# Kernel optimization log

Measured on AMD Instinct MI355X. Metric: run time of the kernel, lower is better.

## Reference

```python
import jax, jax.numpy as jnp
import numpy as np

VOCAB, B, T, E, H, C = 50000, 1024, 120, 50, 300, 5
FORGET_BIAS = 1.0  # tf.nn.rnn_cell.LSTMCell default


def setup_inputs() -> dict:
    key = jax.random.key(0)
    ks = jax.random.split(key, 8)
    tokens = jax.random.randint(ks[0], (B, T, 1), 0, VOCAB, dtype=jnp.int32)
    labels = jax.random.randint(ks[1], (B, T), 0, C, dtype=jnp.int32)
    mask = jax.random.randint(ks[2], (B, T), 0, 2, dtype=jnp.int32).astype(bool)
    embeddings = jax.random.normal(ks[3], (VOCAB, E), dtype=jnp.float32) * 0.1
    Wx = jax.random.normal(ks[4], (E, 4 * H), dtype=jnp.float32) * (1.0 / np.sqrt(E))
    Wh = jax.random.normal(ks[5], (H, 4 * H), dtype=jnp.float32) * (1.0 / np.sqrt(H))
    b = jnp.zeros((4 * H,), dtype=jnp.float32)
    U = jax.random.normal(ks[6], (H, C), dtype=jnp.float32) * (1.0 / np.sqrt(H))
    b2 = jnp.zeros((C,), dtype=jnp.float32)
    return {"tokens": tokens, "labels": labels, "mask": mask,
            "embeddings": embeddings, "Wx": Wx, "Wh": Wh, "b": b, "U": U, "b2": b2}


def reference(tokens, labels, mask, embeddings, Wx, Wh, b, U, b2):
    # Embedding lookup: (B, T, n_features=1) -> (B, T, E)
    x = embeddings[tokens[..., 0]]

    def step(carry, xt):
        c, h = carry
        z = xt @ Wx + h @ Wh + b           # (B, 4H), gate order i, j, f, o
        i, j, f, o = jnp.split(z, 4, axis=-1)
        c_new = jax.nn.sigmoid(f + FORGET_BIAS) * c + jax.nn.sigmoid(i) * jnp.tanh(j)
        h_new = jax.nn.sigmoid(o) * jnp.tanh(c_new)
        return (c_new, h_new), h_new

    nb = x.shape[0]
    c0 = jnp.zeros((nb, H), dtype=x.dtype)
    h0 = jnp.zeros((nb, H), dtype=x.dtype)
    _, hs = jax.lax.scan(step, (c0, h0), jnp.swapaxes(x, 0, 1))  # (T, B, H)
    hs = jnp.swapaxes(hs, 0, 1)                                   # (B, T, H)

    logits = hs @ U + b2                                          # (B, T, C)
    logp = jax.nn.log_softmax(logits, axis=-1)
    ce = -jnp.take_along_axis(logp, labels[..., None].astype(jnp.int32), axis=-1)[..., 0]
    m = mask.astype(ce.dtype)
    loss = jnp.sum(ce * m) / jnp.sum(m)  # mean over unmasked tokens
    return loss
```

## Files before the change

kernel.cpp:

```cpp
#include <hip/hip_runtime.h>
#include <hip/hip_bf16.h>
#include <math.h>

#define NBATCH 1024
#define NT 120
#define NE 50
#define NH 300
#define NC 5
#define GH 1200
#define NKPAD 352
#define NSTRIP 15
#define HS 20
#define SCOL 80
#define NGRP 16
#define BB 64
#define ASTR 376
#define WSTR 376
#define ZSTR 84
#define HBSTR 304
#define HCH 76
#define NCHUNK 4800

typedef __attribute__((ext_vector_type(8))) short short8;
typedef __attribute__((ext_vector_type(4))) float f32x4;
typedef __attribute__((ext_vector_type(2))) unsigned short us2;

static __device__ __forceinline__ float bf2f(unsigned short u) {
    unsigned int x = ((unsigned int)u) << 16;
    return __builtin_bit_cast(float, x);
}
static __device__ __forceinline__ unsigned short f2bf(float f) {
    __hip_bfloat16 h = __float2bfloat16(f);
    return __builtin_bit_cast(unsigned short, h);
}

static __device__ __forceinline__ float sigmoid_fast(float x) {
    return __builtin_amdgcn_rcpf(1.f + __expf(-x));
}
static __device__ __forceinline__ float tanh_fast(float x) {
    return 1.f - 2.f * __builtin_amdgcn_rcpf(1.f + __expf(2.f * x));
}

__global__ __launch_bounds__(256)
void wswz_kernel(const float* __restrict__ Wx, const float* __restrict__ Wh,
                 unsigned short* __restrict__ Wswz)
{
    int idx = blockIdx.x * 256 + threadIdx.x;
    if (idx >= NSTRIP * SCOL * NKPAD) return;
    int s = idx / (SCOL * NKPAD);
    int r = idx % (SCOL * NKPAD);
    int j = r / NKPAD, k = r % NKPAD;
    int col = (j & 3) * NH + s * HS + (j >> 2);
    float v = 0.f;
    if (k < NH)           v = Wh[k * GH + col];
    else if (k < NH + NE) v = Wx[(k - NH) * GH + col];
    Wswz[idx] = f2bf(v);
}

__device__ __forceinline__ void load_h(const unsigned short* __restrict__ hb,
                                       int b0, unsigned short* A_s, int tid)
{
    const unsigned long long* src =
        (const unsigned long long*)(hb + (size_t)b0 * HBSTR);
    unsigned long long v[19];
#pragma unroll
    for (int m = 0; m < 19; ++m) {
        const int idx = tid + 256 * m;
        if (idx < NCHUNK) {
            const int row = idx / 75, j = idx % 75;
            v[m] = __hip_atomic_load(src + (size_t)row * HCH + j,
                                     __ATOMIC_RELAXED, __HIP_MEMORY_SCOPE_AGENT);
        }
    }
#pragma unroll
    for (int m = 0; m < 19; ++m) {
        const int idx = tid + 256 * m;
        if (idx < NCHUNK) {
            const int row = idx / 75, j = idx % 75;
            *(unsigned long long*)(A_s + row * ASTR + j * 4) = v[m];
        }
    }
}

__device__ __forceinline__ void store_h(unsigned short* hb, int b0, int st,
                                        const unsigned short* h_stage, int tid)
{
#pragma unroll
    for (int m = 0; m < 2; ++m) {
        const int c = tid + m * 256;
        if (c < 320) {
            const int row = c / 5, j = c % 5;
            unsigned long long val =
                *(const unsigned long long*)(h_stage + row * HS + j * 4);
            unsigned long long* p = (unsigned long long*)
                (hb + (size_t)(b0 + row) * HBSTR + st * HS + j * 4);
            __hip_atomic_store(p, val, __ATOMIC_RELAXED,
                               __HIP_MEMORY_SCOPE_AGENT);
        }
    }
}

__device__ __forceinline__ void load_x(const int* __restrict__ tokens,
                                       const float* __restrict__ emb,
                                       int b0, int t, unsigned short* A_s, int tid)
{
    const int row = tid >> 2, q = tid & 3;
    const int tok = tokens[(b0 + row) * NT + t];
    const float* er = emb + (size_t)tok * NE;
    unsigned short* dst = A_s + row * ASTR + NH;
    for (int m = 0; m < 7; ++m) {
        int f = q + 4 * m;
        if (f < 25) {
            float2 v = *(const float2*)(er + f * 2);
            us2 o; o.x = f2bf(v.x); o.y = f2bf(v.y);
            *(us2*)(dst + f * 2) = o;
        }
    }
}

__device__ __forceinline__ void ce_phase0(bool doCE, int r0, int nr,
        const unsigned short* A_s, const float* U_s, float* llds, int tid)
{
    if (!doCE || tid >= 192) return;
    for (int item = tid; item < nr * 50; item += 192) {
        int i = item / 50, rem = item % 50, c = rem / 10, q = rem % 10;
        const unsigned short* ar = A_s + (r0 + i) * ASTR + q * 30;
        const float* up = U_s + q * 30 * NC + c;
        float acc = 0.f;
#pragma unroll
        for (int k = 0; k < 30; ++k) acc += bf2f(ar[k]) * up[k * NC];
        llds[i * 50 + c * 10 + q] = acc;
    }
}

__device__ __forceinline__ void ce_final(bool doCE, int tc, int b0, int r0,
        int nr, const float* b2r, const int* __restrict__ labels,
        const int* __restrict__ mask, float* __restrict__ ce_arr,
        const float* llds, int tid)
{
    if (!doCE || tid >= nr) return;
    const float* pp = llds + tid * 50;
    float L[5];
#pragma unroll
    for (int c = 0; c < 5; ++c) {
        float sum = 0.f;
#pragma unroll
        for (int q = 0; q < 10; ++q) sum += pp[c * 10 + q];
        L[c] = sum + b2r[c];
    }
    float m = fmaxf(fmaxf(fmaxf(L[0], L[1]), fmaxf(L[2], L[3])), L[4]);
    float ssum = expf(L[0]-m)+expf(L[1]-m)+expf(L[2]-m)+expf(L[3]-m)+expf(L[4]-m);
    float lse = m + logf(ssum);
    int bidx = b0 + r0 + tid;
    int lab = labels[bidx * NT + tc];
    int mk  = mask[bidx * NT + tc];
    ce_arr[bidx * NT + tc] = mk ? (lse - L[lab]) : 0.f;
}

__global__ __launch_bounds__(256, 1)
void lstm_persist(const int* __restrict__ tokens,
                  const int* __restrict__ labels,
                  const int* __restrict__ mask,
                  const float* __restrict__ emb,
                  const float* __restrict__ bias,
                  const float* __restrict__ U,
                  const float* __restrict__ b2,
                  const unsigned short* __restrict__ Wswz,
                  unsigned short* __restrict__ hbuf,
                  float* __restrict__ ce_arr,
                  int* __restrict__ flags)
{
    __shared__ unsigned short A_s[BB * ASTR];
    __shared__ unsigned short W_s[SCOL * WSTR];
    __shared__ __align__(16) unsigned short h_stage[BB * HS];
    __shared__ float z_s[BB * ZSTR];
    __shared__ float c_s[BB * HS];
    __shared__ float U_s[NH * NC];
    __shared__ float b_s[SCOL];
    __shared__ float llds[5 * 50];

    const int tid  = threadIdx.x;
    const int g    = blockIdx.x & 15;
    const int s    = blockIdx.x >> 4;
    const int b0   = g * BB;
    const int wave = tid >> 6;
    const int lane = tid & 63;
    const int c15  = lane & 15;
    const int kq   = lane >> 4;
    const int r0   = (s * BB) / NSTRIP;
    const int r1   = ((s + 1) * BB) / NSTRIP;
    const int nr   = r1 - r0;

    for (int idx = tid; idx < SCOL * 44; idx += 256) {
        int j = idx / 44, ch = idx % 44;
        *(uint4*)(W_s + j * WSTR + ch * 8) =
            *(const uint4*)(Wswz + (size_t)s * SCOL * NKPAD + j * NKPAD + ch * 8);
    }
    for (int idx = tid; idx < BB * NH; idx += 256) {
        int row = idx / NH, k = idx % NH;
        A_s[row * ASTR + k] = 0;
    }
    for (int idx = tid; idx < BB * 26; idx += 256) {
        int row = idx / 26, k = 350 + idx % 26;
        A_s[row * ASTR + k] = 0;
    }
    for (int idx = tid; idx < BB * HS; idx += 256) c_s[idx] = 0.f;
    for (int idx = tid; idx < NH * NC; idx += 256) U_s[idx] = U[idx];
    if (tid < SCOL) b_s[tid] = bias[(tid & 3) * NH + s * HS + (tid >> 2)];
    float b2r[5];
#pragma unroll
    for (int c = 0; c < 5; ++c) b2r[c] = b2[c];
    load_x(tokens, emb, b0, 0, A_s, tid);
    __syncthreads();

    const unsigned short* Ab = A_s + (wave * 16 + c15) * ASTR + kq * 8;
    const unsigned short* Wb = W_s + c15 * WSTR + kq * 8;

    for (int t = 0; t < NT; ++t) {
        f32x4 acc[5];
#pragma unroll
        for (int n = 0; n < 5; ++n) acc[n] = (f32x4){0.f, 0.f, 0.f, 0.f};
#pragma unroll
        for (int ks = 0; ks < 11; ++ks) {
            short8 av = *(const short8*)(Ab + ks * 32);
#pragma unroll
            for (int n = 0; n < 5; ++n) {
                short8 bv = *(const short8*)(Wb + n * 16 * WSTR + ks * 32);
                acc[n] = __builtin_amdgcn_mfma_f32_16x16x32_bf16(av, bv, acc[n], 0, 0, 0);
            }
        }
#pragma unroll
        for (int n = 0; n < 5; ++n)
#pragma unroll
            for (int j = 0; j < 4; ++j)
                z_s[(wave * 16 + kq * 4 + j) * ZSTR + n * 16 + c15] = acc[n][j];
        __syncthreads();

        if (t + 1 < NT) load_x(tokens, emb, b0, t + 1, A_s, tid);
#pragma unroll
        for (int ii = 0; ii < 5; ++ii) {
            int idx = tid * 5 + ii;
            int row = idx / HS, h = idx % HS;
            f32x4 z4 = *(f32x4*)(z_s + row * ZSTR + h * 4);
            float zi = z4[0] + b_s[4 * h + 0];
            float zj = z4[1] + b_s[4 * h + 1];
            float zf = z4[2] + b_s[4 * h + 2];
            float zo = z4[3] + b_s[4 * h + 3];
            float co = c_s[idx];
            float fg = sigmoid_fast(zf + 1.f);
            float ig = sigmoid_fast(zi);
            float og = sigmoid_fast(zo);
            float cn = fg * co + ig * tanh_fast(zj);
            float hn = og * tanh_fast(cn);
            c_s[idx] = cn;
            h_stage[idx] = f2bf(hn);
        }
        __syncthreads();

        unsigned short* hb = hbuf + (size_t)(t & 1) * (NBATCH * HBSTR);
        store_h(hb, b0, s, h_stage, tid);
        ce_phase0(t >= 1, r0, nr, A_s, U_s, llds, tid);
        asm volatile("s_waitcnt vmcnt(0)" ::: "memory");
        __syncthreads();

        if (tid == 0)
            __hip_atomic_store(flags + (size_t)(t * NGRP + g) * 16 + s, 1,
                               __ATOMIC_RELAXED, __HIP_MEMORY_SCOPE_AGENT);
        if (tid >= 192) {
            if (tid < 192 + NSTRIP) {
                const int* fp = flags + (size_t)(t * NGRP + g) * 16 + (tid - 192);
                int fv = 0; int gu = 0;
                do {
                    fv = __hip_atomic_load(fp, __ATOMIC_RELAXED,
                                           __HIP_MEMORY_SCOPE_AGENT);
                    if (!fv) __builtin_amdgcn_s_sleep(1);
                } while (!fv && ++gu < (1 << 17));
            }
        } else {
            ce_final(t >= 1, t - 1, b0, r0, nr, b2r, labels, mask,
                     ce_arr, llds, tid);
        }
        __syncthreads();

        load_h(hb, b0, A_s, tid);
        __syncthreads();
    }

    ce_phase0(true, r0, nr, A_s, U_s, llds, tid);
    __syncthreads();
    ce_final(true, NT - 1, b0, r0, nr, b2r, labels, mask, ce_arr, llds, tid);
}

__global__ __launch_bounds__(256)
void reduce1_kernel(const float* __restrict__ ce_arr,
                    const int* __restrict__ mask,
                    float* __restrict__ pce, float* __restrict__ pm)
{
    __shared__ float s_ce[256];
    __shared__ float s_m[256];
    const int tid = threadIdx.x;
    const int lo = blockIdx.x * 480;
    float ac = 0.f, am = 0.f;
    for (int i = lo + tid; i < lo + 480; i += 256) {
        ac += ce_arr[i];
        am += (float)mask[i];
    }
    s_ce[tid] = ac; s_m[tid] = am;
    __syncthreads();
    for (int r = 128; r > 0; r >>= 1) {
        if (tid < r) { s_ce[tid] += s_ce[tid + r]; s_m[tid] += s_m[tid + r]; }
        __syncthreads();
    }
    if (tid == 0) { pce[blockIdx.x] = s_ce[0]; pm[blockIdx.x] = s_m[0]; }
}

__global__ __launch_bounds__(256)
void reduce2_kernel(const float* __restrict__ pce,
                    const float* __restrict__ pm,
                    float* __restrict__ out)
{
    __shared__ float s_ce[256];
    __shared__ float s_m[256];
    const int tid = threadIdx.x;
    s_ce[tid] = pce[tid];
    s_m[tid]  = pm[tid];
    __syncthreads();
    for (int r = 128; r > 0; r >>= 1) {
        if (tid < r) { s_ce[tid] += s_ce[tid + r]; s_m[tid] += s_m[tid + r]; }
        __syncthreads();
    }
    if (tid == 0) out[0] = s_ce[0] / s_m[0];
}

extern "C" void kernel_launch(void* const* d_in, const int* in_sizes, int n_in,
                              void* d_out, int out_size, void* d_ws, size_t ws_size,
                              hipStream_t stream)
{
    const int*   tokens = (const int*)d_in[0];
    const int*   labels = (const int*)d_in[1];
    const int*   mask   = (const int*)d_in[2];
    const float* emb    = (const float*)d_in[3];
    const float* Wx     = (const float*)d_in[4];
    const float* Wh     = (const float*)d_in[5];
    const float* bias   = (const float*)d_in[6];
    const float* U      = (const float*)d_in[7];
    const float* b2     = (const float*)d_in[8];

    char* wsb = (char*)d_ws;
    unsigned short* Wswz = (unsigned short*)wsb;
    unsigned short* hbuf = (unsigned short*)(wsb + 844800);
    float* ce    = (float*)(wsb + 2089984);
    float* pce   = (float*)(wsb + 2581504);
    float* pm    = (float*)(wsb + 2582528);
    int*   flags = (int*)(wsb + 2583552);

    hipMemsetAsync(flags, 0, 122880, stream);
    wswz_kernel<<<(NSTRIP * SCOL * NKPAD + 255) / 256, 256, 0, stream>>>(Wx, Wh, Wswz);
    lstm_persist<<<NGRP * NSTRIP, 256, 0, stream>>>(
        tokens, labels, mask, emb, bias, U, b2, Wswz, hbuf, ce, flags);
    reduce1_kernel<<<256, 256, 0, stream>>>(ce, mask, pce, pm);
    reduce2_kernel<<<1, 256, 0, stream>>>(pce, pm, (float*)d_out);
}
```

Before: 670.1 us.

## Replace block-wide barriers with per-wave decoupled sync and wave-level flags

Each wave now owns 16 batch rows end to end: it writes z, runs the gate math, stores its h slice, publishes a per-wave monotonic step counter, and polls only the matching waves of the other strips before reloading its own h rows. All __syncthreads in the time loop become wave-local LDS waits. The cross-entropy projection is fused into a per-wave shuffle reduction, and the per-step flag array is replaced by counters, which shrinks the memset. This removes block barriers and lets waves progress independently, at the cost of 4x more flag traffic and polling. Ordering of h stores relative to flag stores still relies on an explicit vmcnt wait with relaxed atomics.

```diff
diff --git a/kernel.cpp b/kernel.cpp
--- a/kernel.cpp
+++ b/kernel.cpp
@@ -19,10 +19,11 @@
 #define ZSTR 84
 #define HBSTR 304
 #define HCH 76
-#define NCHUNK 4800
+typedef unsigned long long ull;
 
 typedef __attribute__((ext_vector_type(8))) short short8;
 typedef __attribute__((ext_vector_type(4))) float f32x4;
+typedef __attribute__((ext_vector_type(4))) unsigned short us4;
 typedef __attribute__((ext_vector_type(2))) unsigned short us2;
 
 static __device__ __forceinline__ float bf2f(unsigned short u) {
@@ -33,13 +34,15 @@
     __hip_bfloat16 h = __float2bfloat16(f);
     return __builtin_bit_cast(unsigned short, h);
 }
-
 static __device__ __forceinline__ float sigmoid_fast(float x) {
     return __builtin_amdgcn_rcpf(1.f + __expf(-x));
 }
 static __device__ __forceinline__ float tanh_fast(float x) {
     return 1.f - 2.f * __builtin_amdgcn_rcpf(1.f + __expf(2.f * x));
 }
+#define LGKM_FENCE() do { \
+    asm volatile("s_waitcnt lgkmcnt(0)" ::: "memory"); \
+    __builtin_amdgcn_sched_barrier(0); } while (0)
 
 __global__ __launch_bounds__(256)
 void wswz_kernel(const float* __restrict__ Wx, const float* __restrict__ Wh,
@@ -57,57 +60,15 @@
     Wswz[idx] = f2bf(v);
 }
 
-__device__ __forceinline__ void load_h(const unsigned short* __restrict__ hb,
-                                       int b0, unsigned short* A_s, int tid)
-{
-    const unsigned long long* src =
-        (const unsigned long long*)(hb + (size_t)b0 * HBSTR);
-    unsigned long long v[19];
-#pragma unroll
-    for (int m = 0; m < 19; ++m) {
-        const int idx = tid + 256 * m;
-        if (idx < NCHUNK) {
-            const int row = idx / 75, j = idx % 75;
-            v[m] = __hip_atomic_load(src + (size_t)row * HCH + j,
-                                     __ATOMIC_RELAXED, __HIP_MEMORY_SCOPE_AGENT);
-        }
-    }
-#pragma unroll
-    for (int m = 0; m < 19; ++m) {
-        const int idx = tid + 256 * m;
-        if (idx < NCHUNK) {
-            const int row = idx / 75, j = idx % 75;
-            *(unsigned long long*)(A_s + row * ASTR + j * 4) = v[m];
-        }
-    }
-}
-
-__device__ __forceinline__ void store_h(unsigned short* hb, int b0, int st,
-                                        const unsigned short* h_stage, int tid)
-{
-#pragma unroll
-    for (int m = 0; m < 2; ++m) {
-        const int c = tid + m * 256;
-        if (c < 320) {
-            const int row = c / 5, j = c % 5;
-            unsigned long long val =
-                *(const unsigned long long*)(h_stage + row * HS + j * 4);
-            unsigned long long* p = (unsigned long long*)
-                (hb + (size_t)(b0 + row) * HBSTR + st * HS + j * 4);
-            __hip_atomic_store(p, val, __ATOMIC_RELAXED,
-                               __HIP_MEMORY_SCOPE_AGENT);
-        }
-    }
-}
-
-__device__ __forceinline__ void load_x(const int* __restrict__ tokens,
-                                       const float* __restrict__ emb,
-                                       int b0, int t, unsigned short* A_s, int tid)
-{
-    const int row = tid >> 2, q = tid & 3;
+__device__ __forceinline__ void load_x_wave(const int* __restrict__ tokens,
+        const float* __restrict__ emb, int b0, int w, int t,
+        unsigned short* A_s, int lane)
+{
+    const int row = w * 16 + (lane >> 2), q = lane & 3;
     const int tok = tokens[(b0 + row) * NT + t];
     const float* er = emb + (size_t)tok * NE;
     unsigned short* dst = A_s + row * ASTR + NH;
+#pragma unroll
     for (int m = 0; m < 7; ++m) {
         int f = q + 4 * m;
         if (f < 25) {
@@ -118,43 +79,89 @@
     }
 }
 
-__device__ __forceinline__ void ce_phase0(bool doCE, int r0, int nr,
-        const unsigned short* A_s, const float* U_s, float* llds, int tid)
-{
-    if (!doCE || tid >= 192) return;
-    for (int item = tid; item < nr * 50; item += 192) {
-        int i = item / 50, rem = item % 50, c = rem / 10, q = rem % 10;
-        const unsigned short* ar = A_s + (r0 + i) * ASTR + q * 30;
-        const float* up = U_s + q * 30 * NC + c;
-        float acc = 0.f;
-#pragma unroll
-        for (int k = 0; k < 30; ++k) acc += bf2f(ar[k]) * up[k * NC];
-        llds[i * 50 + c * 10 + q] = acc;
-    }
-}
-
-__device__ __forceinline__ void ce_final(bool doCE, int tc, int b0, int r0,
-        int nr, const float* b2r, const int* __restrict__ labels,
-        const int* __restrict__ mask, float* __restrict__ ce_arr,
-        const float* llds, int tid)
-{
-    if (!doCE || tid >= nr) return;
-    const float* pp = llds + tid * 50;
-    float L[5];
-#pragma unroll
-    for (int c = 0; c < 5; ++c) {
-        float sum = 0.f;
-#pragma unroll
-        for (int q = 0; q < 10; ++q) sum += pp[c * 10 + q];
-        L[c] = sum + b2r[c];
-    }
-    float m = fmaxf(fmaxf(fmaxf(L[0], L[1]), fmaxf(L[2], L[3])), L[4]);
-    float ssum = expf(L[0]-m)+expf(L[1]-m)+expf(L[2]-m)+expf(L[3]-m)+expf(L[4]-m);
-    float lse = m + logf(ssum);
-    int bidx = b0 + r0 + tid;
-    int lab = labels[bidx * NT + tc];
-    int mk  = mask[bidx * NT + tc];
-    ce_arr[bidx * NT + tc] = mk ? (lse - L[lab]) : 0.f;
+__device__ __forceinline__ void store_h_wave(unsigned short* hb, int b0,
+        int s, int w, const unsigned short* h_stage, int lane)
+{
+#pragma unroll
+    for (int m = 0; m < 2; ++m) {
+        const int c = lane + 64 * m;
+        if (c < 80) {
+            const int rl = c / 5, j = c % 5;
+            ull val = *(const ull*)(h_stage + (w * 16 + rl) * HS + j * 4);
+            ull* p = (ull*)(hb + (size_t)(b0 + w * 16 + rl) * HBSTR
+                            + s * HS + j * 4);
+            __hip_atomic_store(p, val, __ATOMIC_RELAXED,
+                               __HIP_MEMORY_SCOPE_AGENT);
+        }
+    }
+}
+
+__device__ __forceinline__ void load_h_wave(const unsigned short* __restrict__ hb,
+        int b0, int w, unsigned short* A_s, int lane)
+{
+    const ull* src = (const ull*)hb;
+    ull v[19];
+#pragma unroll
+    for (int m = 0; m < 19; ++m) {
+        const int idx = lane + 64 * m;
+        if (idx < 1200) {
+            const int rl = idx / 75, j = idx % 75;
+            v[m] = __hip_atomic_load(src + (size_t)(b0 + w * 16 + rl) * HCH + j,
+                                     __ATOMIC_RELAXED, __HIP_MEMORY_SCOPE_AGENT);
+        }
+    }
+#pragma unroll
+    for (int m = 0; m < 19; ++m) {
+        const int idx = lane + 64 * m;
+        if (idx < 1200) {
+            const int rl = idx / 75, j = idx % 75;
+            *(ull*)(A_s + (w * 16 + rl) * ASTR + j * 4) = v[m];
+        }
+    }
+}
+
+__device__ __forceinline__ void ce_wave(bool doCE, int tc, int b0, int lo,
+        int hi, const unsigned short* A_s, const float* U_s,
+        const float* b2r, const int* __restrict__ labels,
+        const int* __restrict__ mask, float* __restrict__ ce_arr, int lane)
+{
+    if (!doCE || lo >= hi) return;
+    const int ridx = lane >> 2, part = lane & 3;
+    const int row = lo + ridx;
+    const bool act = (row < hi) && (ridx < hi - lo);
+    float L0 = 0.f, L1 = 0.f, L2 = 0.f, L3 = 0.f, L4 = 0.f;
+    if (act) {
+        const int k0 = part * 76;
+        const int n4 = (part < 3) ? 19 : 18;
+        const unsigned short* ar = A_s + row * ASTR + k0;
+        for (int c4 = 0; c4 < n4; ++c4) {
+            us4 hv4 = *(const us4*)(ar + c4 * 4);
+#pragma unroll
+            for (int e = 0; e < 4; ++e) {
+                float hv = bf2f(hv4[e]);
+                const float* up = U_s + (k0 + c4 * 4 + e) * NC;
+                L0 += hv * up[0]; L1 += hv * up[1]; L2 += hv * up[2];
+                L3 += hv * up[3]; L4 += hv * up[4];
+            }
+        }
+    }
+    L0 += __shfl_xor(L0, 1, 64); L0 += __shfl_xor(L0, 2, 64);
+    L1 += __shfl_xor(L1, 1, 64); L1 += __shfl_xor(L1, 2, 64);
+    L2 += __shfl_xor(L2, 1, 64); L2 += __shfl_xor(L2, 2, 64);
+    L3 += __shfl_xor(L3, 1, 64); L3 += __shfl_xor(L3, 2, 64);
+    L4 += __shfl_xor(L4, 1, 64); L4 += __shfl_xor(L4, 2, 64);
+    if (act && part == 0) {
+        float L[5] = { L0 + b2r[0], L1 + b2r[1], L2 + b2r[2],
+                       L3 + b2r[3], L4 + b2r[4] };
+        float m = fmaxf(fmaxf(fmaxf(L[0], L[1]), fmaxf(L[2], L[3])), L[4]);
+        float ssum = expf(L[0]-m)+expf(L[1]-m)+expf(L[2]-m)
+                   + expf(L[3]-m)+expf(L[4]-m);
+        float lse = m + logf(ssum);
+        int bidx = b0 + row;
+        int lab = labels[bidx * NT + tc];
+        int mk  = mask[bidx * NT + tc];
+        ce_arr[bidx * NT + tc] = mk ? (lse - L[lab]) : 0.f;
+    }
 }
 
 __global__ __launch_bounds__(256, 1)
@@ -177,19 +184,19 @@
     __shared__ float c_s[BB * HS];
     __shared__ float U_s[NH * NC];
     __shared__ float b_s[SCOL];
-    __shared__ float llds[5 * 50];
 
     const int tid  = threadIdx.x;
     const int g    = blockIdx.x & 15;
     const int s    = blockIdx.x >> 4;
     const int b0   = g * BB;
-    const int wave = tid >> 6;
+    const int w    = tid >> 6;
     const int lane = tid & 63;
     const int c15  = lane & 15;
     const int kq   = lane >> 4;
     const int r0   = (s * BB) / NSTRIP;
     const int r1   = ((s + 1) * BB) / NSTRIP;
-    const int nr   = r1 - r0;
+    const int lo   = max(r0, w * 16);
+    const int hi   = min(r1, w * 16 + 16);
 
     for (int idx = tid; idx < SCOL * 44; idx += 256) {
         int j = idx / 44, ch = idx % 44;
@@ -210,10 +217,10 @@
     float b2r[5];
 #pragma unroll
     for (int c = 0; c < 5; ++c) b2r[c] = b2[c];
-    load_x(tokens, emb, b0, 0, A_s, tid);
+    load_x_wave(tokens, emb, b0, w, 0, A_s, lane);
     __syncthreads();
 
-    const unsigned short* Ab = A_s + (wave * 16 + c15) * ASTR + kq * 8;
+    const unsigned short* Ab = A_s + (w * 16 + c15) * ASTR + kq * 8;
     const unsigned short* Wb = W_s + c15 * WSTR + kq * 8;
 
     for (int t = 0; t < NT; ++t) {
@@ -233,62 +240,66 @@
         for (int n = 0; n < 5; ++n)
 #pragma unroll
             for (int j = 0; j < 4; ++j)
-                z_s[(wave * 16 + kq * 4 + j) * ZSTR + n * 16 + c15] = acc[n][j];
-        __syncthreads();
-
-        if (t + 1 < NT) load_x(tokens, emb, b0, t + 1, A_s, tid);
+                z_s[(w * 16 + kq * 4 + j) * ZSTR + n * 16 + c15] = acc[n][j];
+        LGKM_FENCE();
+
+        if (t + 1 < NT) load_x_wave(tokens, emb, b0, w, t + 1, A_s, lane);
+
 #pragma unroll
         for (int ii = 0; ii < 5; ++ii) {
-            int idx = tid * 5 + ii;
-            int row = idx / HS, h = idx % HS;
-            f32x4 z4 = *(f32x4*)(z_s + row * ZSTR + h * 4);
+            int idxl = lane * 5 + ii;
+            int rl = idxl / HS, h = idxl % HS;
+            int grow = w * 16 + rl;
+            f32x4 z4 = *(f32x4*)(z_s + grow * ZSTR + h * 4);
             float zi = z4[0] + b_s[4 * h + 0];
             float zj = z4[1] + b_s[4 * h + 1];
             float zf = z4[2] + b_s[4 * h + 2];
             float zo = z4[3] + b_s[4 * h + 3];
-            float co = c_s[idx];
+            int cidx = w * 320 + idxl;
+            float co = c_s[cidx];
             float fg = sigmoid_fast(zf + 1.f);
             float ig = sigmoid_fast(zi);
             float og = sigmoid_fast(zo);
             float cn = fg * co + ig * tanh_fast(zj);
             float hn = og * tanh_fast(cn);
-            c_s[idx] = cn;
-            h_stage[idx] = f2bf(hn);
-        }
-        __syncthreads();
+            c_s[cidx] = cn;
+            h_stage[cidx] = f2bf(hn);
+        }
+        LGKM_FENCE();
 
         unsigned short* hb = hbuf + (size_t)(t & 1) * (NBATCH * HBSTR);
-        store_h(hb, b0, s, h_stage, tid);
-        ce_phase0(t >= 1, r0, nr, A_s, U_s, llds, tid);
+        store_h_wave(hb, b0, s, w, h_stage, lane);
         asm volatile("s_waitcnt vmcnt(0)" ::: "memory");
-        __syncthreads();
-
-        if (tid == 0)
-            __hip_atomic_store(flags + (size_t)(t * NGRP + g) * 16 + s, 1,
+
+        if (lane == 0)
+            __hip_atomic_store(flags + g * 64 + s * 4 + w, t + 1,
                                __ATOMIC_RELAXED, __HIP_MEMORY_SCOPE_AGENT);
-        if (tid >= 192) {
-            if (tid < 192 + NSTRIP) {
-                const int* fp = flags + (size_t)(t * NGRP + g) * 16 + (tid - 192);
-                int fv = 0; int gu = 0;
-                do {
-                    fv = __hip_atomic_load(fp, __ATOMIC_RELAXED,
-                                           __HIP_MEMORY_SCOPE_AGENT);
-                    if (!fv) __builtin_amdgcn_s_sleep(1);
-                } while (!fv && ++gu < (1 << 17));
+
+        ce_wave(t >= 1, t - 1, b0, lo, hi, A_s, U_s, b2r,
+                labels, mask, ce_arr, lane);
+
+        {
+            const int* fbase = flags + g * 64 + w;
+            int done = (lane >= NSTRIP);
+            int gu = 0;
+            while (true) {
+                if (!done) {
+                    int fv = __hip_atomic_load(fbase + lane * 4,
+                                               __ATOMIC_RELAXED,
+                                               __HIP_MEMORY_SCOPE_AGENT);
+                    done = (fv >= t + 1);
+                }
+                if (__ballot(done) == ~0ull) break;
+                if (++gu > (1 << 20)) break;
+                __builtin_amdgcn_s_sleep(2);
             }
-        } else {
-            ce_final(t >= 1, t - 1, b0, r0, nr, b2r, labels, mask,
-                     ce_arr, llds, tid);
-        }
-        __syncthreads();
-
-        load_h(hb, b0, A_s, tid);
-        __syncthreads();
-    }
-
-    ce_phase0(true, r0, nr, A_s, U_s, llds, tid);
-    __syncthreads();
-    ce_final(true, NT - 1, b0, r0, nr, b2r, labels, mask, ce_arr, llds, tid);
+        }
+
+        load_h_wave(hb, b0, w, A_s, lane);
+        LGKM_FENCE();
+    }
+
+    ce_wave(true, NT - 1, b0, lo, hi, A_s, U_s, b2r, labels, mask, ce_arr, lane);
 }
 
 __global__ __launch_bounds__(256)
@@ -354,7 +365,7 @@
     float* pm    = (float*)(wsb + 2582528);
     int*   flags = (int*)(wsb + 2583552);
 
-    hipMemsetAsync(flags, 0, 122880, stream);
+    hipMemsetAsync(flags, 0, 4096, stream);
     wswz_kernel<<<(NSTRIP * SCOL * NKPAD + 255) / 256, 256, 0, stream>>>(Wx, Wh, Wswz);
     lstm_persist<<<NGRP * NSTRIP, 256, 0, stream>>>(
         tokens, labels, mask, emb, bias, U, b2, Wswz, hbuf, ce, flags);
```

Result: slower. 1.188 ms (+77.3%).

## Overlap per-strip flag waits with h loads and copy own strip locally

Applied to the files above, without the earlier changes.

The old step waited on all 15 strip flags, hit a barrier, then had every thread load the whole hidden state. Now each 16-thread group handles one strip. It waits on that strip's flag (one lane polls and broadcasts) and loads that strip's h slice into shared memory as soon as it is ready. The block's own strip is copied directly from h_stage without a global round trip. This removes a barrier and overlaps slow-arriving strips with loads of ready ones. It moves the CE final work to the last 16 threads, which assumes nr never exceeds 16, and raises the spin limit.

```diff
diff --git a/kernel.cpp b/kernel.cpp
--- a/kernel.cpp
+++ b/kernel.cpp
@@ -18,8 +18,7 @@
 #define WSTR 376
 #define ZSTR 84
 #define HBSTR 304
-#define HCH 76
-#define NCHUNK 4800
+typedef unsigned long long ull;
 
 typedef __attribute__((ext_vector_type(8))) short short8;
 typedef __attribute__((ext_vector_type(4))) float f32x4;
@@ -33,7 +32,6 @@
     __hip_bfloat16 h = __float2bfloat16(f);
     return __builtin_bit_cast(unsigned short, h);
 }
-
 static __device__ __forceinline__ float sigmoid_fast(float x) {
     return __builtin_amdgcn_rcpf(1.f + __expf(-x));
 }
@@ -57,31 +55,6 @@
     Wswz[idx] = f2bf(v);
 }
 
-__device__ __forceinline__ void load_h(const unsigned short* __restrict__ hb,
-                                       int b0, unsigned short* A_s, int tid)
-{
-    const unsigned long long* src =
-        (const unsigned long long*)(hb + (size_t)b0 * HBSTR);
-    unsigned long long v[19];
-#pragma unroll
-    for (int m = 0; m < 19; ++m) {
-        const int idx = tid + 256 * m;
-        if (idx < NCHUNK) {
-            const int row = idx / 75, j = idx % 75;
-            v[m] = __hip_atomic_load(src + (size_t)row * HCH + j,
-                                     __ATOMIC_RELAXED, __HIP_MEMORY_SCOPE_AGENT);
-        }
-    }
-#pragma unroll
-    for (int m = 0; m < 19; ++m) {
-        const int idx = tid + 256 * m;
-        if (idx < NCHUNK) {
-            const int row = idx / 75, j = idx % 75;
-            *(unsigned long long*)(A_s + row * ASTR + j * 4) = v[m];
-        }
-    }
-}
-
 __device__ __forceinline__ void store_h(unsigned short* hb, int b0, int st,
                                         const unsigned short* h_stage, int tid)
 {
@@ -90,10 +63,8 @@
         const int c = tid + m * 256;
         if (c < 320) {
             const int row = c / 5, j = c % 5;
-            unsigned long long val =
-                *(const unsigned long long*)(h_stage + row * HS + j * 4);
-            unsigned long long* p = (unsigned long long*)
-                (hb + (size_t)(b0 + row) * HBSTR + st * HS + j * 4);
+            ull val = *(const ull*)(h_stage + row * HS + j * 4);
+            ull* p = (ull*)(hb + (size_t)(b0 + row) * HBSTR + st * HS + j * 4);
             __hip_atomic_store(p, val, __ATOMIC_RELAXED,
                                __HIP_MEMORY_SCOPE_AGENT);
         }
@@ -136,10 +107,10 @@
 __device__ __forceinline__ void ce_final(bool doCE, int tc, int b0, int r0,
         int nr, const float* b2r, const int* __restrict__ labels,
         const int* __restrict__ mask, float* __restrict__ ce_arr,
-        const float* llds, int tid)
-{
-    if (!doCE || tid >= nr) return;
-    const float* pp = llds + tid * 50;
+        const float* llds, int idx)
+{
+    if (!doCE || idx >= nr) return;
+    const float* pp = llds + idx * 50;
     float L[5];
 #pragma unroll
     for (int c = 0; c < 5; ++c) {
@@ -151,7 +122,7 @@
     float m = fmaxf(fmaxf(fmaxf(L[0], L[1]), fmaxf(L[2], L[3])), L[4]);
     float ssum = expf(L[0]-m)+expf(L[1]-m)+expf(L[2]-m)+expf(L[3]-m)+expf(L[4]-m);
     float lse = m + logf(ssum);
-    int bidx = b0 + r0 + tid;
+    int bidx = b0 + r0 + idx;
     int lab = labels[bidx * NT + tc];
     int mk  = mask[bidx * NT + tc];
     ce_arr[bidx * NT + tc] = mk ? (lse - L[lab]) : 0.f;
@@ -190,6 +161,8 @@
     const int r0   = (s * BB) / NSTRIP;
     const int r1   = ((s + 1) * BB) / NSTRIP;
     const int nr   = r1 - r0;
+    const int sp   = tid >> 4;
+    const int kk   = tid & 15;
 
     for (int idx = tid; idx < SCOL * 44; idx += 256) {
         int j = idx / 44, ch = idx % 44;
@@ -266,23 +239,48 @@
         if (tid == 0)
             __hip_atomic_store(flags + (size_t)(t * NGRP + g) * 16 + s, 1,
                                __ATOMIC_RELAXED, __HIP_MEMORY_SCOPE_AGENT);
-        if (tid >= 192) {
-            if (tid < 192 + NSTRIP) {
-                const int* fp = flags + (size_t)(t * NGRP + g) * 16 + (tid - 192);
+        if (tid < 240) {
+            if (sp == s) {
+#pragma unroll
+                for (int r4 = 0; r4 < 4; ++r4) {
+                    int row = kk * 4 + r4;
+#pragma unroll
+                    for (int j = 0; j < 5; ++j)
+                        *(ull*)(A_s + row * ASTR + s * HS + j * 4) =
+                            *(const ull*)(h_stage + row * HS + j * 4);
+                }
+            } else {
+                const int lead = lane & ~15;
+                const int* fp = flags + (size_t)(t * NGRP + g) * 16 + sp;
                 int fv = 0; int gu = 0;
                 do {
-                    fv = __hip_atomic_load(fp, __ATOMIC_RELAXED,
-                                           __HIP_MEMORY_SCOPE_AGENT);
-                    if (!fv) __builtin_amdgcn_s_sleep(1);
-                } while (!fv && ++gu < (1 << 17));
+                    int lv = 0;
+                    if (lane == lead)
+                        lv = __hip_atomic_load(fp, __ATOMIC_RELAXED,
+                                               __HIP_MEMORY_SCOPE_AGENT);
+                    fv = __shfl(lv, lead, 64);
+                    if (!fv) __builtin_amdgcn_s_sleep(2);
+                } while (!fv && ++gu < (1 << 20));
+                ull v[20];
+#pragma unroll
+                for (int r4 = 0; r4 < 4; ++r4)
+#pragma unroll
+                    for (int j = 0; j < 5; ++j)
+                        v[r4 * 5 + j] = __hip_atomic_load(
+                            (const ull*)(hb + (size_t)(b0 + kk * 4 + r4) * HBSTR
+                                         + sp * HS + j * 4),
+                            __ATOMIC_RELAXED, __HIP_MEMORY_SCOPE_AGENT);
+#pragma unroll
+                for (int r4 = 0; r4 < 4; ++r4)
+#pragma unroll
+                    for (int j = 0; j < 5; ++j)
+                        *(ull*)(A_s + (kk * 4 + r4) * ASTR + sp * HS + j * 4) =
+                            v[r4 * 5 + j];
             }
         } else {
             ce_final(t >= 1, t - 1, b0, r0, nr, b2r, labels, mask,
-                     ce_arr, llds, tid);
-        }
-        __syncthreads();
-
-        load_h(hb, b0, A_s, tid);
+                     ce_arr, llds, tid - 240);
+        }
         __syncthreads();
     }
 
```

New measurement: 900.8 us. +34.4%, slower.
